# Optimization experiments

Measured on AMD Instinct MI355X. Metric: run time of the kernel, lower is better.

Reference implementation:

```python
import jax, jax.numpy as jnp
import numpy as np

B, N, D = 16, 2048, 64


def setup_inputs() -> dict:
    key = jax.random.key(0)
    kq, kk, kv = jax.random.split(key, 3)
    queries = jax.random.normal(kq, (B, N, D), dtype=jnp.float32)
    keys = jax.random.normal(kk, (B, N, D), dtype=jnp.float32)
    values = jax.random.normal(kv, (B, N, D), dtype=jnp.float32)
    return {"queries": queries, "keys": keys, "values": values}


def reference(queries, keys, values):
    d = queries.shape[-1]
    scale = 1.0 / jnp.sqrt(jnp.asarray(d, dtype=queries.dtype))
    # scores: [B, N, N] = Q @ K^T / sqrt(d)
    scores = jnp.einsum("bqd,bkd->bqk", queries, keys) * scale
    attn = jax.nn.softmax(scores, axis=-1)
    # dropout prob = 0.0 -> identity (inference-faithful)
    out = jnp.einsum("bqk,bkd->bqd", attn, values)
    return out
```

## Files before the change

### kernel.cpp

```cpp
#include <hip/hip_runtime.h>

typedef __attribute__((ext_vector_type(8)))  __bf16 bf16x8;
typedef __attribute__((ext_vector_type(4)))  __bf16 bf16x4;
typedef __attribute__((ext_vector_type(16))) float  f32x16;
typedef __attribute__((ext_vector_type(4)))  float  f32x4;

#define B_    16
#define N_    2048
#define D_    64
#define QBLK  128
#define KVBLK 32
#define NT    (N_ / KVBLK)
#define NG    4
#define TPG   (NT / NG)

#define VSTR    72
#define SLOT_SZ 8704
#define GRP_SZ  (2 * SLOT_SZ)
#define SMEM_SZ (4 * GRP_SZ)

static __device__ __forceinline__ float fast_exp2(float x) {
#if __has_builtin(__builtin_amdgcn_exp2f)
    return __builtin_amdgcn_exp2f(x);
#else
    return __expf(x * 0.6931471805599453f);
#endif
}

__global__ __attribute__((amdgpu_waves_per_eu(4, 4))) __launch_bounds__(1024)
void attn_fwd(const float* __restrict__ Qp, const float* __restrict__ Kp,
              const float* __restrict__ Vp, float* __restrict__ Op)
{
    __shared__ __align__(16) char smem[SMEM_SZ];

    const int tid  = threadIdx.x;
    const int g    = tid >> 8;
    const int tg   = tid & 255;
    const int lane = tid & 63;
    const int w    = (tid >> 6) & 3;
    const int h    = lane >> 5;
    const int qcol = lane & 31;

    const int bx    = blockIdx.x;
    const int batch = ((bx & 7) << 1) | ((bx >> 3) & 1);
    const int qtile = bx >> 4;
    const int q0w   = qtile * QBLK + w * 32;

    const float SL2E = 0.18033688011112042f;
    const size_t bboff = (size_t)batch * (N_ * D_);

    char* gbase = smem + g * GRP_SZ;

    const float* qrow = Qp + bboff + (size_t)(q0w + qcol) * D_ + h * 8;
    bf16x8 qf[4];
#pragma unroll
    for (int m = 0; m < 4; ++m) {
        f32x4 a = *reinterpret_cast<const f32x4*>(qrow + m * 16);
        f32x4 b = *reinterpret_cast<const f32x4*>(qrow + m * 16 + 4);
#pragma unroll
        for (int j = 0; j < 4; ++j) { qf[m][j] = (__bf16)a[j]; qf[m][4 + j] = (__bf16)b[j]; }
    }

    const int krow = tg >> 3,  kcol = (tg & 7) * 8;
    const int vrow = tg & 31,  vcol = (tg >> 5) * 8;
    const float* ksrc0 = Kp + bboff + (size_t)krow * D_ + kcol;
    const float* vsrc0 = Vp + bboff + (size_t)vrow * D_ + vcol;

    f32x4 kr[2], vr[2];
    auto load_tile = [&](int t) {
        const float* ks = ksrc0 + (size_t)t * KVBLK * D_;
        const float* vs = vsrc0 + (size_t)t * KVBLK * D_;
        kr[0] = *reinterpret_cast<const f32x4*>(ks);
        kr[1] = *reinterpret_cast<const f32x4*>(ks + 4);
        vr[0] = *reinterpret_cast<const f32x4*>(vs);
        vr[1] = *reinterpret_cast<const f32x4*>(vs + 4);
    };

    auto write_tile = [&](int b) {
        char* kb = gbase + b * SLOT_SZ;
        char* vb = kb + 4096;
        bf16x8 w0;
#pragma unroll
        for (int j = 0; j < 4; ++j) { w0[j] = (__bf16)kr[0][j]; w0[4 + j] = (__bf16)kr[1][j]; }
        *reinterpret_cast<bf16x8*>(kb + krow * 128 + ((kcol * 2) ^ ((krow & 7) << 4))) = w0;
#pragma unroll 8
        for (int i = 0; i < 8; ++i) {
            const int d = vcol + i;
            *reinterpret_cast<__bf16*>(vb + d * VSTR + vrow * 2) =
                (__bf16)vr[i >> 2][i & 3];
        }
    };

    f32x16 o0, o1;
#pragma unroll
    for (int i = 0; i < 16; ++i) { o0[i] = 0.f; o1[i] = 0.f; }
    float m_run = -1e30f, l_run = 0.f;

    const int kx = (qcol & 7) << 4;

    load_tile(g);
    write_tile(0);
    __syncthreads();

    for (int it = 0; it < TPG; ++it) {
        const int cur = it & 1;
        if (it + 1 < TPG) load_tile(NG * (it + 1) + g);

        const char* kb = gbase + cur * SLOT_SZ;
        const char* vb = kb + 4096;

        f32x16 s;
#pragma unroll
        for (int i = 0; i < 16; ++i) s[i] = 0.f;
        __builtin_amdgcn_s_setprio(1);
#pragma unroll
        for (int m = 0; m < 4; ++m) {
            const int col = m * 32 + h * 16;
            bf16x8 k0 = *reinterpret_cast<const bf16x8*>(kb + qcol * 128 + (col ^ kx));
            s = __builtin_amdgcn_mfma_f32_32x32x16_bf16(k0, qf[m], s, 0, 0, 0);
        }
        __builtin_amdgcn_s_setprio(0);

        float t8[8];
#pragma unroll
        for (int i = 0; i < 8; ++i) t8[i] = fmaxf(s[i], s[8 + i]);
        float t4a = fmaxf(t8[0], t8[1]), t4b = fmaxf(t8[2], t8[3]);
        float t4c = fmaxf(t8[4], t8[5]), t4d = fmaxf(t8[6], t8[7]);
        float tmax = fmaxf(fmaxf(t4a, t4b), fmaxf(t4c, t4d));
        tmax = fmaxf(tmax, __shfl_xor(tmax, 32));

        if (!__all(tmax <= m_run + 16.0f)) {
            const float mnew  = fmaxf(m_run, tmax);
            const float alpha = fast_exp2((m_run - mnew) * SL2E);
            l_run *= alpha;
#pragma unroll
            for (int i = 0; i < 16; ++i) { o0[i] *= alpha; o1[i] *= alpha; }
            m_run = mnew;
        }

        const float nmk = -m_run * SL2E;
        float ps0 = 0.f, ps1 = 0.f, ps2 = 0.f, ps3 = 0.f;
        bf16x8 pfa, pfb;
#pragma unroll
        for (int i = 0; i < 4; ++i) {
            float p0 = fast_exp2(fmaf(s[i],      SL2E, nmk));
            float p1 = fast_exp2(fmaf(s[4 + i],  SL2E, nmk));
            float p2 = fast_exp2(fmaf(s[8 + i],  SL2E, nmk));
            float p3 = fast_exp2(fmaf(s[12 + i], SL2E, nmk));
            ps0 += p0; ps1 += p1; ps2 += p2; ps3 += p3;
            pfa[i] = (__bf16)p0; pfa[4 + i] = (__bf16)p1;
            pfb[i] = (__bf16)p2; pfb[4 + i] = (__bf16)p3;
        }
        l_run += (ps0 + ps1) + (ps2 + ps3);

        __builtin_amdgcn_s_setprio(1);
#pragma unroll
        for (int db = 0; db < 2; ++db) {
            const int drow = db * 32 + qcol;
            const char* vrowp = vb + drow * VSTR;
            f32x16& oo = db ? o1 : o0;
#pragma unroll
            for (int sub = 0; sub < 2; ++sub) {
                const int cb = sub * 32 + h * 8;
                bf16x4 v0 = *reinterpret_cast<const bf16x4*>(vrowp + cb);
                bf16x4 v1 = *reinterpret_cast<const bf16x4*>(vrowp + cb + 16);
                bf16x8 vf;
#pragma unroll
                for (int j = 0; j < 4; ++j) { vf[j] = v0[j]; vf[4 + j] = v1[j]; }
                oo = __builtin_amdgcn_mfma_f32_32x32x16_bf16(vf, sub ? pfb : pfa, oo, 0, 0, 0);
            }
        }
        __builtin_amdgcn_s_setprio(0);

        if (it + 1 < TPG) write_tile(cur ^ 1);
        __syncthreads();
    }

    const float lt = l_run + __shfl_xor(l_run, 32);
    float* mlF  = (float*)smem;
    float* slab = (float*)smem;
    const int q  = w * 32 + qcol;

    if (h == 0) {
        mlF[(g * QBLK + q) * 2]     = m_run;
        mlF[(g * QBLK + q) * 2 + 1] = lt;
    }
    __syncthreads();

    float mg[4], lg[4];
#pragma unroll
    for (int gg = 0; gg < 4; ++gg) {
        mg[gg] = mlF[(gg * QBLK + q) * 2];
        lg[gg] = mlF[(gg * QBLK + q) * 2 + 1];
    }
    const float mm = fmaxf(fmaxf(mg[0], mg[1]), fmaxf(mg[2], mg[3]));
    float L = 0.f;
#pragma unroll
    for (int gg = 0; gg < 4; ++gg) L += fast_exp2((mg[gg] - mm) * SL2E) * lg[gg];
    const float a_self = fast_exp2((m_run - mm) * SL2E);
    const float inv = 1.0f / L;
    __syncthreads();

    const int dl0 = 4 * h;
    auto slab_write = [&](float* sb, const f32x16& oo, int db, float scale) {
#pragma unroll
        for (int r = 0; r < 16; ++r) {
            const int d = db * 32 + (r & 3) + 8 * (r >> 2) + dl0;
            sb[d * 128 + q] = scale * oo[r];
        }
    };
    auto slab_add = [&](const float* sb, f32x16& oo, int db, float scale) {
#pragma unroll
        for (int r = 0; r < 16; ++r) {
            const int d = db * 32 + (r & 3) + 8 * (r >> 2) + dl0;
            oo[r] = fmaf(scale, oo[r], sb[d * 128 + q]);
        }
    };

    if (g == 1) { slab_write(slab, o0, 0, a_self);        slab_write(slab, o1, 1, a_self); }
    if (g == 3) { slab_write(slab + 8192, o0, 0, a_self); slab_write(slab + 8192, o1, 1, a_self); }
    __syncthreads();

    if (g == 0) { slab_add(slab, o0, 0, a_self);        slab_add(slab, o1, 1, a_self); }
    if (g == 2) { slab_add(slab + 8192, o0, 0, a_self); slab_add(slab + 8192, o1, 1, a_self); }
    __syncthreads();

    if (g == 2) { slab_write(slab, o0, 0, 1.0f); slab_write(slab, o1, 1, 1.0f); }
    __syncthreads();

    if (g == 0) {
#pragma unroll
        for (int r = 0; r < 16; ++r) {
            const int d0 = (r & 3) + 8 * (r >> 2) + dl0;
            o0[r] = (o0[r] + slab[d0 * 128 + q]) * inv;
            o1[r] = (o1[r] + slab[(32 + d0) * 128 + q]) * inv;
        }
        float* orow = Op + bboff + (size_t)(q0w + qcol) * D_;
#pragma unroll
        for (int gg8 = 0; gg8 < 4; ++gg8) {
            f32x4 v, v2;
#pragma unroll
            for (int r = 0; r < 4; ++r) { v[r] = o0[4 * gg8 + r]; v2[r] = o1[4 * gg8 + r]; }
            *reinterpret_cast<f32x4*>(orow + gg8 * 8 + 4 * h)      = v;
            *reinterpret_cast<f32x4*>(orow + 32 + gg8 * 8 + 4 * h) = v2;
        }
    }
}

extern "C" void kernel_launch(void* const* d_in, const int* in_sizes, int n_in,
                              void* d_out, int out_size, void* d_ws, size_t ws_size,
                              hipStream_t stream) {
    const float* Q = (const float*)d_in[0];
    const float* K = (const float*)d_in[1];
    const float* V = (const float*)d_in[2];
    float* O = (float*)d_out;
    dim3 grid(256), block(1024);
    hipLaunchKernelGGL(attn_fwd, grid, block, 0, stream, Q, K, V, O);
}
```

Before: 39.63 us.

## Switch to 16x16 MFMA tiles with 64-query blocks and two KV groups

Halves the query tile per block to 64 rows and splits the KV sequence across two groups instead of four, launching 512 blocks of 512 threads. Both attention matmuls move from 32x32x16 to 16x16x32 bf16 MFMA, with matching register layouts for the scores, the softmax row reductions and the PV accumulators. The cross-group merge collapses to a single LDS exchange between two groups, replacing the multi-stage slab reduction. The aim is to cut the merge and sync overhead and to balance work across CUs. In exchange, global K/V traffic doubles because each K/V tile is now reused by fewer query rows.

```diff
diff --git a/kernel.cpp b/kernel.cpp
--- a/kernel.cpp
+++ b/kernel.cpp
@@ -2,22 +2,22 @@
 
 typedef __attribute__((ext_vector_type(8)))  __bf16 bf16x8;
 typedef __attribute__((ext_vector_type(4)))  __bf16 bf16x4;
-typedef __attribute__((ext_vector_type(16))) float  f32x16;
 typedef __attribute__((ext_vector_type(4)))  float  f32x4;
 
 #define B_    16
 #define N_    2048
 #define D_    64
-#define QBLK  128
+#define QBLK  64
 #define KVBLK 32
+#define NG    2
 #define NT    (N_ / KVBLK)
-#define NG    4
 #define TPG   (NT / NG)
 
 #define VSTR    72
-#define SLOT_SZ 8704
+#define KSZ     4096
+#define SLOT_SZ (KSZ + 64 * VSTR)
 #define GRP_SZ  (2 * SLOT_SZ)
-#define SMEM_SZ (4 * GRP_SZ)
+#define SMEM_SZ (NG * GRP_SZ)
 
 static __device__ __forceinline__ float fast_exp2(float x) {
 #if __has_builtin(__builtin_amdgcn_exp2f)
@@ -27,38 +27,38 @@
 #endif
 }
 
-__global__ __attribute__((amdgpu_waves_per_eu(4, 4))) __launch_bounds__(1024)
+__global__ __attribute__((amdgpu_waves_per_eu(4, 4))) __launch_bounds__(512)
 void attn_fwd(const float* __restrict__ Qp, const float* __restrict__ Kp,
               const float* __restrict__ Vp, float* __restrict__ Op)
 {
     __shared__ __align__(16) char smem[SMEM_SZ];
 
     const int tid  = threadIdx.x;
-    const int g    = tid >> 8;
+    const int wv   = tid >> 6;
+    const int g    = wv >> 2;
+    const int w    = wv & 3;
+    const int lane = tid & 63;
+    const int hh   = lane >> 4;
+    const int qr   = lane & 15;
     const int tg   = tid & 255;
-    const int lane = tid & 63;
-    const int w    = (tid >> 6) & 3;
-    const int h    = lane >> 5;
-    const int qcol = lane & 31;
 
     const int bx    = blockIdx.x;
     const int batch = ((bx & 7) << 1) | ((bx >> 3) & 1);
     const int qtile = bx >> 4;
-    const int q0w   = qtile * QBLK + w * 32;
+    const int q0w   = qtile * QBLK + w * 16;
 
     const float SL2E = 0.18033688011112042f;
     const size_t bboff = (size_t)batch * (N_ * D_);
-
     char* gbase = smem + g * GRP_SZ;
 
-    const float* qrow = Qp + bboff + (size_t)(q0w + qcol) * D_ + h * 8;
-    bf16x8 qf[4];
-#pragma unroll
-    for (int m = 0; m < 4; ++m) {
-        f32x4 a = *reinterpret_cast<const f32x4*>(qrow + m * 16);
-        f32x4 b = *reinterpret_cast<const f32x4*>(qrow + m * 16 + 4);
-#pragma unroll
-        for (int j = 0; j < 4; ++j) { qf[m][j] = (__bf16)a[j]; qf[m][4 + j] = (__bf16)b[j]; }
+    const float* qrow = Qp + bboff + (size_t)(q0w + qr) * D_ + hh * 8;
+    bf16x8 qf[2];
+#pragma unroll
+    for (int kc = 0; kc < 2; ++kc) {
+        f32x4 a = *reinterpret_cast<const f32x4*>(qrow + kc * 32);
+        f32x4 b = *reinterpret_cast<const f32x4*>(qrow + kc * 32 + 4);
+#pragma unroll
+        for (int j = 0; j < 4; ++j) { qf[kc][j] = (__bf16)a[j]; qf[kc][4 + j] = (__bf16)b[j]; }
     }
 
     const int krow = tg >> 3,  kcol = (tg & 7) * 8;
@@ -78,7 +78,7 @@
 
     auto write_tile = [&](int b) {
         char* kb = gbase + b * SLOT_SZ;
-        char* vb = kb + 4096;
+        char* vb = kb + KSZ;
         bf16x8 w0;
 #pragma unroll
         for (int j = 0; j < 4; ++j) { w0[j] = (__bf16)kr[0][j]; w0[4 + j] = (__bf16)kr[1][j]; }
@@ -91,12 +91,14 @@
         }
     };
 
-    f32x16 o0, o1;
-#pragma unroll
-    for (int i = 0; i < 16; ++i) { o0[i] = 0.f; o1[i] = 0.f; }
+    f32x4 o[4];
+#pragma unroll
+    for (int dc = 0; dc < 4; ++dc)
+#pragma unroll
+        for (int r = 0; r < 4; ++r) o[dc][r] = 0.f;
     float m_run = -1e30f, l_run = 0.f;
 
-    const int kx = (qcol & 7) << 4;
+    const int kx = (lane & 7) << 4;
 
     load_tile(g);
     write_tile(0);
@@ -107,26 +109,26 @@
         if (it + 1 < TPG) load_tile(NG * (it + 1) + g);
 
         const char* kb = gbase + cur * SLOT_SZ;
-        const char* vb = kb + 4096;
-
-        f32x16 s;
-#pragma unroll
-        for (int i = 0; i < 16; ++i) s[i] = 0.f;
+        const char* vb = kb + KSZ;
+
+        f32x4 s0, s1;
+#pragma unroll
+        for (int r = 0; r < 4; ++r) { s0[r] = 0.f; s1[r] = 0.f; }
         __builtin_amdgcn_s_setprio(1);
 #pragma unroll
-        for (int m = 0; m < 4; ++m) {
-            const int col = m * 32 + h * 16;
-            bf16x8 k0 = *reinterpret_cast<const bf16x8*>(kb + qcol * 128 + (col ^ kx));
-            s = __builtin_amdgcn_mfma_f32_32x32x16_bf16(k0, qf[m], s, 0, 0, 0);
+        for (int kc = 0; kc < 2; ++kc) {
+            const int off = (kc * 64 + 16 * hh) ^ kx;
+            bf16x8 k0 = *reinterpret_cast<const bf16x8*>(kb + qr * 128        + off);
+            bf16x8 k1 = *reinterpret_cast<const bf16x8*>(kb + (16 + qr) * 128 + off);
+            s0 = __builtin_amdgcn_mfma_f32_16x16x32_bf16(k0, qf[kc], s0, 0, 0, 0);
+            s1 = __builtin_amdgcn_mfma_f32_16x16x32_bf16(k1, qf[kc], s1, 0, 0, 0);
         }
         __builtin_amdgcn_s_setprio(0);
 
-        float t8[8];
-#pragma unroll
-        for (int i = 0; i < 8; ++i) t8[i] = fmaxf(s[i], s[8 + i]);
-        float t4a = fmaxf(t8[0], t8[1]), t4b = fmaxf(t8[2], t8[3]);
-        float t4c = fmaxf(t8[4], t8[5]), t4d = fmaxf(t8[6], t8[7]);
-        float tmax = fmaxf(fmaxf(t4a, t4b), fmaxf(t4c, t4d));
+        float e0 = fmaxf(s0[0], s1[0]), e1 = fmaxf(s0[1], s1[1]);
+        float e2 = fmaxf(s0[2], s1[2]), e3 = fmaxf(s0[3], s1[3]);
+        float tmax = fmaxf(fmaxf(e0, e1), fmaxf(e2, e3));
+        tmax = fmaxf(tmax, __shfl_xor(tmax, 16));
         tmax = fmaxf(tmax, __shfl_xor(tmax, 32));
 
         if (!__all(tmax <= m_run + 16.0f)) {
@@ -134,41 +136,34 @@
             const float alpha = fast_exp2((m_run - mnew) * SL2E);
             l_run *= alpha;
 #pragma unroll
-            for (int i = 0; i < 16; ++i) { o0[i] *= alpha; o1[i] *= alpha; }
+            for (int dc = 0; dc < 4; ++dc)
+#pragma unroll
+                for (int r = 0; r < 4; ++r) o[dc][r] *= alpha;
             m_run = mnew;
         }
 
         const float nmk = -m_run * SL2E;
-        float ps0 = 0.f, ps1 = 0.f, ps2 = 0.f, ps3 = 0.f;
-        bf16x8 pfa, pfb;
-#pragma unroll
-        for (int i = 0; i < 4; ++i) {
-            float p0 = fast_exp2(fmaf(s[i],      SL2E, nmk));
-            float p1 = fast_exp2(fmaf(s[4 + i],  SL2E, nmk));
-            float p2 = fast_exp2(fmaf(s[8 + i],  SL2E, nmk));
-            float p3 = fast_exp2(fmaf(s[12 + i], SL2E, nmk));
-            ps0 += p0; ps1 += p1; ps2 += p2; ps3 += p3;
-            pfa[i] = (__bf16)p0; pfa[4 + i] = (__bf16)p1;
-            pfb[i] = (__bf16)p2; pfb[4 + i] = (__bf16)p3;
-        }
-        l_run += (ps0 + ps1) + (ps2 + ps3);
+        float ps0 = 0.f, ps1 = 0.f;
+        bf16x8 pf;
+#pragma unroll
+        for (int j = 0; j < 4; ++j) {
+            float p0 = fast_exp2(fmaf(s0[j], SL2E, nmk));
+            float p1 = fast_exp2(fmaf(s1[j], SL2E, nmk));
+            ps0 += p0; ps1 += p1;
+            pf[j] = (__bf16)p0; pf[4 + j] = (__bf16)p1;
+        }
+        l_run += ps0 + ps1;
 
         __builtin_amdgcn_s_setprio(1);
 #pragma unroll
-        for (int db = 0; db < 2; ++db) {
-            const int drow = db * 32 + qcol;
-            const char* vrowp = vb + drow * VSTR;
-            f32x16& oo = db ? o1 : o0;
-#pragma unroll
-            for (int sub = 0; sub < 2; ++sub) {
-                const int cb = sub * 32 + h * 8;
-                bf16x4 v0 = *reinterpret_cast<const bf16x4*>(vrowp + cb);
-                bf16x4 v1 = *reinterpret_cast<const bf16x4*>(vrowp + cb + 16);
-                bf16x8 vf;
-#pragma unroll
-                for (int j = 0; j < 4; ++j) { vf[j] = v0[j]; vf[4 + j] = v1[j]; }
-                oo = __builtin_amdgcn_mfma_f32_32x32x16_bf16(vf, sub ? pfb : pfa, oo, 0, 0, 0);
-            }
+        for (int dc = 0; dc < 4; ++dc) {
+            const char* vp = vb + (dc * 16 + qr) * VSTR + 8 * hh;
+            bf16x4 v0 = *reinterpret_cast<const bf16x4*>(vp);
+            bf16x4 v1 = *reinterpret_cast<const bf16x4*>(vp + 32);
+            bf16x8 vf;
+#pragma unroll
+            for (int j = 0; j < 4; ++j) { vf[j] = v0[j]; vf[4 + j] = v1[j]; }
+            o[dc] = __builtin_amdgcn_mfma_f32_16x16x32_bf16(vf, pf, o[dc], 0, 0, 0);
         }
         __builtin_amdgcn_s_setprio(0);
 
@@ -176,73 +171,41 @@
         __syncthreads();
     }
 
-    const float lt = l_run + __shfl_xor(l_run, 32);
-    float* mlF  = (float*)smem;
-    float* slab = (float*)smem;
-    const int q  = w * 32 + qcol;
-
-    if (h == 0) {
-        mlF[(g * QBLK + q) * 2]     = m_run;
-        mlF[(g * QBLK + q) * 2 + 1] = lt;
+    float lt = l_run + __shfl_xor(l_run, 16);
+    lt += __shfl_xor(lt, 32);
+
+    float* slabO = (float*)smem;
+    float* mlF   = slabO + 4096;
+    const int slot = (w * 64 + lane) * 16;
+
+    if (g == 1) {
+#pragma unroll
+        for (int dc = 0; dc < 4; ++dc)
+            *reinterpret_cast<f32x4*>(slabO + slot + dc * 4) = o[dc];
+        if (hh == 0) {
+            mlF[(w * 16 + qr) * 2]     = m_run;
+            mlF[(w * 16 + qr) * 2 + 1] = lt;
+        }
     }
     __syncthreads();
 
-    float mg[4], lg[4];
-#pragma unroll
-    for (int gg = 0; gg < 4; ++gg) {
-        mg[gg] = mlF[(gg * QBLK + q) * 2];
-        lg[gg] = mlF[(gg * QBLK + q) * 2 + 1];
-    }
-    const float mm = fmaxf(fmaxf(mg[0], mg[1]), fmaxf(mg[2], mg[3]));
-    float L = 0.f;
-#pragma unroll
-    for (int gg = 0; gg < 4; ++gg) L += fast_exp2((mg[gg] - mm) * SL2E) * lg[gg];
-    const float a_self = fast_exp2((m_run - mm) * SL2E);
-    const float inv = 1.0f / L;
-    __syncthreads();
-
-    const int dl0 = 4 * h;
-    auto slab_write = [&](float* sb, const f32x16& oo, int db, float scale) {
-#pragma unroll
-        for (int r = 0; r < 16; ++r) {
-            const int d = db * 32 + (r & 3) + 8 * (r >> 2) + dl0;
-            sb[d * 128 + q] = scale * oo[r];
-        }
-    };
-    auto slab_add = [&](const float* sb, f32x16& oo, int db, float scale) {
-#pragma unroll
-        for (int r = 0; r < 16; ++r) {
-            const int d = db * 32 + (r & 3) + 8 * (r >> 2) + dl0;
-            oo[r] = fmaf(scale, oo[r], sb[d * 128 + q]);
-        }
-    };
-
-    if (g == 1) { slab_write(slab, o0, 0, a_self);        slab_write(slab, o1, 1, a_self); }
-    if (g == 3) { slab_write(slab + 8192, o0, 0, a_self); slab_write(slab + 8192, o1, 1, a_self); }
-    __syncthreads();
-
-    if (g == 0) { slab_add(slab, o0, 0, a_self);        slab_add(slab, o1, 1, a_self); }
-    if (g == 2) { slab_add(slab + 8192, o0, 0, a_self); slab_add(slab + 8192, o1, 1, a_self); }
-    __syncthreads();
-
-    if (g == 2) { slab_write(slab, o0, 0, 1.0f); slab_write(slab, o1, 1, 1.0f); }
-    __syncthreads();
-
     if (g == 0) {
-#pragma unroll
-        for (int r = 0; r < 16; ++r) {
-            const int d0 = (r & 3) + 8 * (r >> 2) + dl0;
-            o0[r] = (o0[r] + slab[d0 * 128 + q]) * inv;
-            o1[r] = (o1[r] + slab[(32 + d0) * 128 + q]) * inv;
-        }
-        float* orow = Op + bboff + (size_t)(q0w + qcol) * D_;
-#pragma unroll
-        for (int gg8 = 0; gg8 < 4; ++gg8) {
-            f32x4 v, v2;
-#pragma unroll
-            for (int r = 0; r < 4; ++r) { v[r] = o0[4 * gg8 + r]; v2[r] = o1[4 * gg8 + r]; }
-            *reinterpret_cast<f32x4*>(orow + gg8 * 8 + 4 * h)      = v;
-            *reinterpret_cast<f32x4*>(orow + 32 + gg8 * 8 + 4 * h) = v2;
+        const float m1 = mlF[(w * 16 + qr) * 2];
+        const float l1 = mlF[(w * 16 + qr) * 2 + 1];
+        const float mm = fmaxf(m_run, m1);
+        const float a0 = fast_exp2((m_run - mm) * SL2E);
+        const float a1 = fast_exp2((m1 - mm) * SL2E);
+        const float inv = 1.0f / (a0 * lt + a1 * l1);
+
+        float* orow = Op + bboff + (size_t)(q0w + qr) * D_;
+#pragma unroll
+        for (int dc = 0; dc < 4; ++dc) {
+            const f32x4 os = *reinterpret_cast<const f32x4*>(slabO + slot + dc * 4);
+            f32x4 v;
+#pragma unroll
+            for (int r = 0; r < 4; ++r)
+                v[r] = (a0 * o[dc][r] + a1 * os[r]) * inv;
+            *reinterpret_cast<f32x4*>(orow + dc * 16 + 4 * hh) = v;
         }
     }
 }
@@ -254,6 +217,6 @@
     const float* K = (const float*)d_in[1];
     const float* V = (const float*)d_in[2];
     float* O = (float*)d_out;
-    dim3 grid(256), block(1024);
+    dim3 grid(512), block(512);
     hipLaunchKernelGGL(attn_fwd, grid, block, 0, stream, Q, K, V, O);
 }
```

New measurement: 46.54 us. +17.4%, slower.
